# Optimization experiments

Hardware: AMD Instinct MI355X
Metric: run time of the kernel (lower is better)

Reference implementation:

```python
import jax, jax.numpy as jnp
import numpy as np

N_NODES = 100000
N_CLIQUES = 50000
N_EDGES = 1600000
D_IN = 128
D_OUT = 128


def setup_inputs() -> dict:
    key = jax.random.key(0)
    k1, k2, k3, k4, k5, k6 = jax.random.split(key, 6)
    x = jax.random.normal(k1, (N_NODES, D_IN), dtype=jnp.float32)
    x_clique = jax.random.normal(k2, (N_CLIQUES, D_IN), dtype=jnp.float32)
    node_idx = jax.random.randint(k3, (N_EDGES,), 0, N_NODES, dtype=jnp.int64)
    clique_idx = jax.random.randint(k4, (N_EDGES,), 0, N_CLIQUES, dtype=jnp.int64)
    node2clique_index = jnp.stack([node_idx, clique_idx], axis=0)
    # Linear(in, out): weight [out, in], bias [out]
    W = jax.random.normal(k5, (D_OUT, D_IN), dtype=jnp.float32) * (1.0 / np.sqrt(D_IN))
    b = jax.random.normal(k6, (D_OUT,), dtype=jnp.float32) * 0.01
    return {"x": x, "x_clique": x_clique, "node2clique_index": node2clique_index, "W": W, "b": b}


def reference(x, x_clique, node2clique_index, W, b):
    node_idx = node2clique_index[0]
    clique_idx = node2clique_index[1]
    n_nodes = x.shape[0]
    gathered = x_clique[clique_idx]                                   # [E, D_in]
    summed = jax.ops.segment_sum(gathered, node_idx, num_segments=n_nodes)  # [N, D_in]
    count = jax.ops.segment_sum(
        jnp.ones((gathered.shape[0],), dtype=x_clique.dtype), node_idx, num_segments=n_nodes
    )
    mean = summed / jnp.maximum(count, 1.0)[:, None]                  # scatter-mean, count clamped like torch_scatter
    out = mean @ W.T + b                                              # Linear
    return out
```

## Files before the change

### kernel.cpp

```cpp
#include <hip/hip_runtime.h>


typedef short bf16x8 __attribute__((ext_vector_type(8)));
typedef float f32x4  __attribute__((ext_vector_type(4)));
typedef float f32x2  __attribute__((ext_vector_type(2)));

#define BK_SHIFT 8
#define NB_MAX 512
#define BCUR_STRIDE 16
#define RAWCAP 4608
#define PADCAP 6400
#define FCHUNK 4096

__device__ inline ushort f2b(float f) {
    union { float f; uint u; } v; v.f = f;
    uint r = v.u + 0x7FFFu + ((v.u >> 16) & 1u);
    return (ushort)(r >> 16);
}
__device__ inline float blo(uint v) { union { uint u; float f; } x; x.u = v << 16;        return x.f; }
__device__ inline float bhi(uint v) { union { uint u; float f; } x; x.u = v & 0xFFFF0000u; return x.f; }

struct FillSM {
    int cnt[NB_MAX];
    int sloc[NB_MAX];
    int gbase[NB_MAX];
    int cur[NB_MAX];
    int wtot[8];
    uint   stage[FCHUNK];
    ushort sbkt[FCHUNK];
};
struct TransSM { ushort wl[128 * 128]; };

__global__ __launch_bounds__(512) void k_front(const float* __restrict__ xc,
                                               const float* __restrict__ W,
                                               ushort* __restrict__ yb, int nc,
                                               const int* __restrict__ nidx,
                                               const int* __restrict__ cidx,
                                               int* __restrict__ bcur,
                                               uint* __restrict__ pairs,
                                               int ne, int gf) {
    __shared__ union USM { FillSM f; TransSM tr; } sm;
    const int t = threadIdx.x;
    const int lane = t & 63, wid = t >> 6;

    if ((int)blockIdx.x < gf) {
        const int e0 = blockIdx.x * FCHUNK;
        const int e1 = min(e0 + FCHUNK, ne);
        sm.f.cnt[t] = 0;
        sm.f.cur[t] = 0;
        __syncthreads();

        int nn[8], cc[8];
        #pragma unroll
        for (int k = 0; k < 8; ++k) {
            int i = e0 + k * 512 + t;
            if (i < e1) {
                nn[k] = nidx[i];
                cc[k] = cidx[i];
                atomicAdd(&sm.f.cnt[nn[k] >> BK_SHIFT], 1);
            } else nn[k] = -1;
        }
        __syncthreads();

        int v = sm.f.cnt[t];
        int inc = v;
        #pragma unroll
        for (int d = 1; d < 64; d <<= 1) { int x = __shfl_up(inc, d); if (lane >= d) inc += x; }
        if (lane == 63) sm.f.wtot[wid] = inc;
        __syncthreads();
        int wpre = 0;
        for (int i = 0; i < wid; ++i) wpre += sm.f.wtot[i];
        int excl = wpre + inc - v;
        sm.f.sloc[t] = excl;
        if (v > 0) sm.f.gbase[t] = t * RAWCAP + atomicAdd(&bcur[t * BCUR_STRIDE], v);
        __syncthreads();

        #pragma unroll
        for (int k = 0; k < 8; ++k) {
            if (nn[k] >= 0) {
                int b = nn[k] >> BK_SHIFT;
                int slot = sm.f.sloc[b] + atomicAdd(&sm.f.cur[b], 1);
                sm.f.stage[slot] = ((uint)(nn[k] & 255) << 16) | (uint)cc[k];
                sm.f.sbkt[slot] = (ushort)b;
            }
        }
        __syncthreads();

        const int m = e1 - e0;
        for (int i = t; i < m; i += 512) {
            int b = sm.f.sbkt[i];
            pairs[(size_t)sm.f.gbase[b] + (i - sm.f.sloc[b])] = sm.f.stage[i];
        }
    } else {
        const int bid = blockIdx.x - gf;
        if (bid == 0 && t < 64)
            reinterpret_cast<uint*>(&yb[(size_t)nc * 128])[t] = 0u;
        for (int i = 0; i < 8; ++i) {
            int idx = (i * 512 + t) * 4;
            float4 w4 = *reinterpret_cast<const float4*>(&W[idx]);
            int o = idx >> 7, k = idx & 127;
            ushort4 h;
            h.x = f2b(w4.x); h.y = f2b(w4.y); h.z = f2b(w4.z); h.w = f2b(w4.w);
            int byte = o * 256 + k * 2;
            byte ^= (o & 7) << 4;
            *reinterpret_cast<ushort4*>(reinterpret_cast<char*>(sm.tr.wl) + byte) = h;
        }
        __syncthreads();

        const int lrow = lane & 15;
        const int lk = lane >> 4;
        for (int g = 0; g < 2; ++g) {
            const int r0 = bid * 256 + g * 128 + wid * 16;
            const bool rowok = (r0 + lrow) < nc;
            const float* arow = &xc[(size_t)(r0 + lrow) * 128];

            bf16x8 afrag[4];
            for (int kb = 0; kb < 4; ++kb) {
                float4 a0 = make_float4(0.f, 0.f, 0.f, 0.f), a1 = a0;
                if (rowok) {
                    int k0 = kb * 32 + lk * 8;
                    a0 = *reinterpret_cast<const float4*>(&arow[k0]);
                    a1 = *reinterpret_cast<const float4*>(&arow[k0 + 4]);
                }
                bf16x8 a;
                a[0] = (short)f2b(a0.x); a[1] = (short)f2b(a0.y);
                a[2] = (short)f2b(a0.z); a[3] = (short)f2b(a0.w);
                a[4] = (short)f2b(a1.x); a[5] = (short)f2b(a1.y);
                a[6] = (short)f2b(a1.z); a[7] = (short)f2b(a1.w);
                afrag[kb] = a;
            }

            for (int ct = 0; ct < 8; ++ct) {
                f32x4 c = {0.f, 0.f, 0.f, 0.f};
                const int o = ct * 16 + lrow;
                #pragma unroll
                for (int kb = 0; kb < 4; ++kb) {
                    int byte = o * 256 + (kb * 32 + lk * 8) * 2;
                    byte ^= (o & 7) << 4;
                    bf16x8 bb = *reinterpret_cast<const bf16x8*>(reinterpret_cast<const char*>(sm.tr.wl) + byte);
                    c = __builtin_amdgcn_mfma_f32_16x16x32_bf16(afrag[kb], bb, c, 0, 0, 0);
                }
                const int orow = r0 + lk * 4;
                #pragma unroll
                for (int j = 0; j < 4; ++j)
                    if (orow + j < nc)
                        yb[(size_t)(orow + j) * 128 + ct * 16 + lrow] = f2b(c[j]);
            }
        }
    }
}

__global__ __launch_bounds__(512) void k_build(const uint* __restrict__ pairs,
                                               const int* __restrict__ bcur,
                                               int* __restrict__ offsets,
                                               int* __restrict__ ncnt,
                                               ushort* __restrict__ edge_dst,
                                               int n_nodes, int nc) {
    __shared__ int arr[256], nexcl[256], cur[256], wtot[4];
    __shared__ int mpad_sh;
    __shared__ ushort scidx[PADCAP];
    const int b = blockIdx.x, t = threadIdx.x;
    const int p0r = b * RAWCAP;
    const int p0e = b * PADCAP;
    const int m = min(bcur[b * BCUR_STRIDE], RAWCAP);
    const int node0 = b << BK_SHIFT;

    if (t < 256) { arr[t] = 0; cur[t] = 0; }
    __syncthreads();
    for (int i = t; i < m; i += 512)
        atomicAdd(&arr[pairs[p0r + i] >> 16], 1);
    __syncthreads();

    int v = 0, pv = 0, inc = 0;
    if (t < 256) {
        v = arr[t];
        pv = (v + 7) & ~7;
        inc = pv;
        #pragma unroll
        for (int d = 1; d < 64; d <<= 1) {
            int x = __shfl_up(inc, d);
            if ((t & 63) >= d) inc += x;
        }
        if ((t & 63) == 63) wtot[t >> 6] = inc;
    }
    __syncthreads();
    if (t < 256) {
        const int wid = t >> 6;
        int wpre = 0;
        for (int i = 0; i < wid; ++i) wpre += wtot[i];
        const int excl = wpre + inc - pv;
        nexcl[t] = excl;
        if (node0 + t < n_nodes) {
            offsets[node0 + t] = p0e + excl;
            ncnt[node0 + t] = v;
        }
        if (t == 255) mpad_sh = excl + pv;
    }
    __syncthreads();

    for (int i = t; i < m; i += 512) {
        uint p = pairs[p0r + i];
        int l = (int)(p >> 16);
        int slot = nexcl[l] + atomicAdd(&cur[l], 1);
        scidx[slot] = (ushort)(p & 0xFFFFu);
    }
    __syncthreads();
    if (t < 256) {
        const int base = nexcl[t];
        for (int k = v; k < pv; ++k)
            scidx[base + k] = (ushort)nc;
    }
    __syncthreads();
    const int mp2 = mpad_sh >> 1;
    uint* ed32 = reinterpret_cast<uint*>(edge_dst);
    const uint* sc32 = reinterpret_cast<const uint*>(scidx);
    const int p0e2 = p0e >> 1;
    for (int i = t; i < mp2; i += 512)
        ed32[p0e2 + i] = sc32[i];
}

__global__ __launch_bounds__(256) void k_reduce(const ushort* __restrict__ yb,
                                                const int* __restrict__ offsets,
                                                const int* __restrict__ ncnt,
                                                const ushort* __restrict__ edge_dst,
                                                const float* __restrict__ bias,
                                                float* __restrict__ out, int n) {
    int gw = (blockIdx.x * blockDim.x + threadIdx.x) >> 6;
    if (gw >= n) return;
    const int lane = threadIdx.x & 63;
    const int eg = lane >> 4;
    const int ch = lane & 15;
    const int gwu = __builtin_amdgcn_readfirstlane(gw);
    const int s = offsets[gwu];
    const int cnt = ncnt[gwu];
    const int rounds = ((cnt + 7) & ~7) >> 2;

    const ushort* ep = edge_dst + s + eg;
    const char* ybase = reinterpret_cast<const char*>(yb) + ch * 16;

    float a0 = 0.f, a1 = 0.f, a2 = 0.f, a3 = 0.f;
    float a4 = 0.f, a5 = 0.f, a6 = 0.f, a7 = 0.f;
    #pragma unroll 2
    for (int r = 0; r < rounds; ++r) {
        uint c = ep[r * 4];
        uint4 v = *reinterpret_cast<const uint4*>(ybase + (size_t)c * 256);
        a0 += blo(v.x); a1 += bhi(v.x);
        a2 += blo(v.y); a3 += bhi(v.y);
        a4 += blo(v.z); a5 += bhi(v.z);
        a6 += blo(v.w); a7 += bhi(v.w);
    }
    a0 += __shfl_xor(a0, 16); a0 += __shfl_xor(a0, 32);
    a1 += __shfl_xor(a1, 16); a1 += __shfl_xor(a1, 32);
    a2 += __shfl_xor(a2, 16); a2 += __shfl_xor(a2, 32);
    a3 += __shfl_xor(a3, 16); a3 += __shfl_xor(a3, 32);
    a4 += __shfl_xor(a4, 16); a4 += __shfl_xor(a4, 32);
    a5 += __shfl_xor(a5, 16); a5 += __shfl_xor(a5, 32);
    a6 += __shfl_xor(a6, 16); a6 += __shfl_xor(a6, 32);
    a7 += __shfl_xor(a7, 16); a7 += __shfl_xor(a7, 32);

    if (lane < 16) {
        const float inv = 1.0f / (float)max(cnt, 1);
        const f32x4 bv0 = *reinterpret_cast<const f32x4*>(&bias[ch * 8]);
        const f32x4 bv1 = *reinterpret_cast<const f32x4*>(&bias[ch * 8 + 4]);
        f32x4 o0, o1;
        o0.x = a0 * inv + bv0.x;
        o0.y = a1 * inv + bv0.y;
        o0.z = a2 * inv + bv0.z;
        o0.w = a3 * inv + bv0.w;
        o1.x = a4 * inv + bv1.x;
        o1.y = a5 * inv + bv1.y;
        o1.z = a6 * inv + bv1.z;
        o1.w = a7 * inv + bv1.w;
        float* orow = &out[(size_t)gw * 128 + ch * 8];
        __builtin_nontemporal_store(o0, reinterpret_cast<f32x4*>(orow));
        __builtin_nontemporal_store(o1, reinterpret_cast<f32x4*>(orow + 4));
    }
}

extern "C" void kernel_launch(void* const* d_in, const int* in_sizes, int n_in,
                              void* d_out, int out_size, void* d_ws, size_t ws_size,
                              hipStream_t stream) {
    const float* xc  = (const float*)d_in[1];
    const int*   n2c = (const int*)d_in[2];
    const float* W   = (const float*)d_in[3];
    const float* b   = (const float*)d_in[4];
    float* out = (float*)d_out;

    const int n_nodes   = in_sizes[0] / 128;
    const int n_cliques = in_sizes[1] / 128;
    const int n_edges   = in_sizes[2] / 2;
    const int* nidx = n2c;
    const int* cidx = n2c + n_edges;
    const int nbucket = (n_nodes + ((1 << BK_SHIFT) - 1)) >> BK_SHIFT;

    char* ws = (char*)d_ws;
    size_t off = 0;
    ushort* yb = (ushort*)(ws + off);     off += (size_t)(n_cliques + 1) * 128 * sizeof(ushort);
    off = (off + 15) & ~(size_t)15;
    uint* pairs = (uint*)(ws + off);      off += (size_t)nbucket * RAWCAP * sizeof(uint);
    ushort* edge_dst = (ushort*)(ws + off); off += (size_t)nbucket * PADCAP * sizeof(ushort);
    off = (off + 15) & ~(size_t)15;
    int* offsets = (int*)(ws + off);      off += (size_t)n_nodes * sizeof(int);
    int* ncnt = (int*)(ws + off);         off += (size_t)n_nodes * sizeof(int);
    int* bcur = (int*)(ws + off);         off += (size_t)NB_MAX * BCUR_STRIDE * sizeof(int);

    (void)hipMemsetAsync(bcur, 0, (size_t)NB_MAX * BCUR_STRIDE * sizeof(int), stream);

    const int gf = (n_edges + FCHUNK - 1) / FCHUNK;
    const int gt = (n_cliques + 255) / 256;
    k_front<<<gf + gt, 512, 0, stream>>>(xc, W, yb, n_cliques, nidx, cidx, bcur,
                                         pairs, n_edges, gf);
    k_build<<<nbucket, 512, 0, stream>>>(pairs, bcur, offsets, ncnt, edge_dst,
                                         n_nodes, n_cliques);
    k_reduce<<<((n_nodes) * 64 + 255) / 256, 256, 0, stream>>>(yb, offsets, ncnt, edge_dst, b, out, n_nodes);
}
```

Before: 104.6 us.

## Reassign reduce lanes to columns and unroll edge gathers sixteen-deep

The per-node reduction kernel previously split the wavefront into four edge groups of sixteen lanes, each loading 16 bytes per edge, and needed cross-lane shuffles at the end. Each lane now owns two output columns and walks every edge of the node. It loads edge indices as packed 32-bit pairs and issues sixteen independent 4-byte gathers per iteration, which raises memory-level parallelism and removes the shuffle reduction. In exchange each gather instruction is narrower (4 bytes per lane instead of 16) and there are more gather instructions per edge, while every lane still does useful work on the output store.

New measurement: 101.3 us. 3.2% less time.

```diff
diff --git a/kernel.cpp b/kernel.cpp
--- a/kernel.cpp
+++ b/kernel.cpp
@@ -228,53 +228,57 @@
     int gw = (blockIdx.x * blockDim.x + threadIdx.x) >> 6;
     if (gw >= n) return;
     const int lane = threadIdx.x & 63;
-    const int eg = lane >> 4;
-    const int ch = lane & 15;
     const int gwu = __builtin_amdgcn_readfirstlane(gw);
     const int s = offsets[gwu];
     const int cnt = ncnt[gwu];
-    const int rounds = ((cnt + 7) & ~7) >> 2;
-
-    const ushort* ep = edge_dst + s + eg;
-    const char* ybase = reinterpret_cast<const char*>(yb) + ch * 16;
-
-    float a0 = 0.f, a1 = 0.f, a2 = 0.f, a3 = 0.f;
-    float a4 = 0.f, a5 = 0.f, a6 = 0.f, a7 = 0.f;
-    #pragma unroll 2
-    for (int r = 0; r < rounds; ++r) {
-        uint c = ep[r * 4];
-        uint4 v = *reinterpret_cast<const uint4*>(ybase + (size_t)c * 256);
-        a0 += blo(v.x); a1 += bhi(v.x);
-        a2 += blo(v.y); a3 += bhi(v.y);
-        a4 += blo(v.z); a5 += bhi(v.z);
-        a6 += blo(v.w); a7 += bhi(v.w);
-    }
-    a0 += __shfl_xor(a0, 16); a0 += __shfl_xor(a0, 32);
-    a1 += __shfl_xor(a1, 16); a1 += __shfl_xor(a1, 32);
-    a2 += __shfl_xor(a2, 16); a2 += __shfl_xor(a2, 32);
-    a3 += __shfl_xor(a3, 16); a3 += __shfl_xor(a3, 32);
-    a4 += __shfl_xor(a4, 16); a4 += __shfl_xor(a4, 32);
-    a5 += __shfl_xor(a5, 16); a5 += __shfl_xor(a5, 32);
-    a6 += __shfl_xor(a6, 16); a6 += __shfl_xor(a6, 32);
-    a7 += __shfl_xor(a7, 16); a7 += __shfl_xor(a7, 32);
-
-    if (lane < 16) {
-        const float inv = 1.0f / (float)max(cnt, 1);
-        const f32x4 bv0 = *reinterpret_cast<const f32x4*>(&bias[ch * 8]);
-        const f32x4 bv1 = *reinterpret_cast<const f32x4*>(&bias[ch * 8 + 4]);
-        f32x4 o0, o1;
-        o0.x = a0 * inv + bv0.x;
-        o0.y = a1 * inv + bv0.y;
-        o0.z = a2 * inv + bv0.z;
-        o0.w = a3 * inv + bv0.w;
-        o1.x = a4 * inv + bv1.x;
-        o1.y = a5 * inv + bv1.y;
-        o1.z = a6 * inv + bv1.z;
-        o1.w = a7 * inv + bv1.w;
-        float* orow = &out[(size_t)gw * 128 + ch * 8];
-        __builtin_nontemporal_store(o0, reinterpret_cast<f32x4*>(orow));
-        __builtin_nontemporal_store(o1, reinterpret_cast<f32x4*>(orow + 4));
-    }
+    const int e = (cnt + 7) & ~7;
+    const uint* edp = reinterpret_cast<const uint*>(edge_dst + s);
+    const char* ybase = reinterpret_cast<const char*>(yb) + lane * 4;
+
+    float ax0 = 0.f, ay0 = 0.f, ax1 = 0.f, ay1 = 0.f;
+    int j = 0, q32 = 0;
+    for (; j + 16 <= e; j += 16) {
+        uint w[8];
+        #pragma unroll
+        for (int q = 0; q < 8; ++q) w[q] = edp[q32 + q];
+        q32 += 8;
+        uint v[16];
+        #pragma unroll
+        for (int q = 0; q < 8; ++q) {
+            uint c0 = w[q] & 0xFFFFu, c1 = w[q] >> 16;
+            v[2 * q]     = *reinterpret_cast<const uint*>(ybase + (size_t)c0 * 256);
+            v[2 * q + 1] = *reinterpret_cast<const uint*>(ybase + (size_t)c1 * 256);
+        }
+        #pragma unroll
+        for (int u = 0; u < 16; u += 2) {
+            ax0 += blo(v[u]);     ay0 += bhi(v[u]);
+            ax1 += blo(v[u + 1]); ay1 += bhi(v[u + 1]);
+        }
+    }
+    if (j < e) {
+        uint w[4];
+        #pragma unroll
+        for (int q = 0; q < 4; ++q) w[q] = edp[q32 + q];
+        uint v[8];
+        #pragma unroll
+        for (int q = 0; q < 4; ++q) {
+            uint c0 = w[q] & 0xFFFFu, c1 = w[q] >> 16;
+            v[2 * q]     = *reinterpret_cast<const uint*>(ybase + (size_t)c0 * 256);
+            v[2 * q + 1] = *reinterpret_cast<const uint*>(ybase + (size_t)c1 * 256);
+        }
+        #pragma unroll
+        for (int u = 0; u < 8; u += 2) {
+            ax0 += blo(v[u]);     ay0 += bhi(v[u]);
+            ax1 += blo(v[u + 1]); ay1 += bhi(v[u + 1]);
+        }
+    }
+    float ax = ax0 + ax1, ay = ay0 + ay1;
+    float inv = 1.0f / (float)max(cnt, 1);
+    f32x2 bv = *reinterpret_cast<const f32x2*>(&bias[lane * 2]);
+    f32x2 o;
+    o.x = ax * inv + bv.x;
+    o.y = ay * inv + bv.y;
+    __builtin_nontemporal_store(o, reinterpret_cast<f32x2*>(&out[(size_t)gw * 128 + lane * 2]));
 }
 
 extern "C" void kernel_launch(void* const* d_in, const int* in_sizes, int n_in,
```
